# Kernel tuning notes

Measured on AMD Instinct MI355X. Metric: run time of the kernel, lower is better.

Reference implementation:

```python
import jax, jax.numpy as jnp
import numpy as np

INPUT_DIM = 1024
MEMORY_DIM = 512
MEMORY_SIZE = 4096
TOPK = 8


def setup_inputs() -> dict:
    key = jax.random.key(0)
    ks = jax.random.split(key, 7)
    query = jax.random.normal(ks[0], (8, 4096, INPUT_DIM), dtype=jnp.float32)
    memory_keys = jax.random.normal(ks[1], (MEMORY_SIZE, MEMORY_DIM), dtype=jnp.float32)
    memory_values = jax.random.normal(ks[2], (MEMORY_SIZE, MEMORY_DIM), dtype=jnp.float32)
    # nn.Linear-style init (uniform +-1/sqrt(fan_in))
    wq = jax.random.uniform(ks[3], (INPUT_DIM, MEMORY_DIM), jnp.float32, -1.0, 1.0) / np.sqrt(INPUT_DIM)
    bq = jax.random.uniform(ks[4], (MEMORY_DIM,), jnp.float32, -1.0, 1.0) / np.sqrt(INPUT_DIM)
    wo = jax.random.uniform(ks[5], (MEMORY_DIM, INPUT_DIM), jnp.float32, -1.0, 1.0) / np.sqrt(MEMORY_DIM)
    bo = jax.random.uniform(ks[6], (INPUT_DIM,), jnp.float32, -1.0, 1.0) / np.sqrt(MEMORY_DIM)
    return {"query": query, "memory_keys": memory_keys, "memory_values": memory_values,
            "wq": wq, "bq": bq, "wo": wo, "bo": bo}


def reference(query, memory_keys, memory_values, wq, bq, wo, bo):
    B, S, D = query.shape
    # Query projection: [B,S,M]
    q = jnp.einsum('bsd,dm->bsm', query, wq) + bq
    # Scores vs memory keys: [B,S,memory_size] (no expand needed)
    scores = jnp.einsum('bsm,km->bsk', q, memory_keys)
    # Top-k selection + softmax over selected scores
    topk_w, topk_idx = jax.lax.top_k(scores, TOPK)           # [B,S,K]
    topk_w = jax.nn.softmax(topk_w, axis=-1)
    # Gather selected memory values: [B,S,K,M]
    top_vals = memory_values[topk_idx]
    mem_out = jnp.einsum('bskm,bsk->bsm', top_vals, topk_w)  # weighted sum
    out = jnp.einsum('bsm,md->bsd', mem_out, wo) + bo
    return out + query
```

## Files before the change

kernel.cpp:

```cpp
#include <hip/hip_runtime.h>
#include <cstdint>

typedef _Float16 f16;
typedef uint32_t u32;
typedef f16 f16x2 __attribute__((ext_vector_type(2)));
typedef f16 f16x8 __attribute__((ext_vector_type(8)));
typedef float f32x4 __attribute__((ext_vector_type(4)));
typedef float f32x16 __attribute__((ext_vector_type(16)));
typedef u32 u32x4 __attribute__((ext_vector_type(4)));

#define NROWS 32768
#define D_IN 1024
#define M_DIM 512
#define NKEYS 4096
#define KTOP 8

__device__ __forceinline__ u32 umax32(u32 a, u32 b) { return a > b ? a : b; }
__device__ __forceinline__ u32 umin32(u32 a, u32 b) { return a < b ? a : b; }

__device__ __forceinline__ void gload_lds16(const void* src, void* dst) {
  __builtin_amdgcn_global_load_lds(
      (const __attribute__((address_space(1))) uint32_t*)src,
      (__attribute__((address_space(3))) uint32_t*)dst, 16, 0, 0);
}

__global__ void prep_kernel(const float* __restrict__ keys, const float* __restrict__ values,
                            const float* __restrict__ wq, const float* __restrict__ wo,
                            f16* __restrict__ keys_h, f16* __restrict__ values_h,
                            f16* __restrict__ wqT, f16* __restrict__ woT) {
  const int b = blockIdx.x, t = threadIdx.x;
  if (b < 2048) {
    const float* src = (b < 1024) ? keys : values;
    f16* dst = (b < 1024) ? keys_h : values_h;
    const int bb = b & 1023;
    const size_t base = (size_t)bb * 2048 + (size_t)t * 8;
    f32x4 a = *(const f32x4*)(src + base);
    f32x4 c2 = *(const f32x4*)(src + base + 4);
    f16x8 o;
    o[0] = (f16)a[0]; o[1] = (f16)a[1]; o[2] = (f16)a[2]; o[3] = (f16)a[3];
    o[4] = (f16)c2[0]; o[5] = (f16)c2[1]; o[6] = (f16)c2[2]; o[7] = (f16)c2[3];
    *(f16x8*)(dst + base) = o;
    return;
  }
  __shared__ float lds[64][65];
  if (b < 2176) {
    const int tb = b - 2048;
    const int td = tb >> 3, tm = tb & 7;
#pragma unroll
    for (int p = 0; p < 16; ++p) {
      const int d_loc = p * 4 + (t >> 6), m_loc = t & 63;
      lds[d_loc][m_loc] = wq[(size_t)(td * 64 + d_loc) * 512 + tm * 64 + m_loc];
    }
    __syncthreads();
#pragma unroll
    for (int p = 0; p < 16; ++p) {
      const int m_loc = p * 4 + (t >> 6), d_loc = t & 63;
      wqT[(size_t)(tm * 64 + m_loc) * 1024 + td * 64 + d_loc] = (f16)lds[d_loc][m_loc];
    }
  } else {
    const int tb = b - 2176;
    const int tmm = tb >> 4, tod = tb & 15;
#pragma unroll
    for (int p = 0; p < 16; ++p) {
      const int m_loc = p * 4 + (t >> 6), od_loc = t & 63;
      lds[m_loc][od_loc] = wo[(size_t)(tmm * 64 + m_loc) * 1024 + tod * 64 + od_loc];
    }
    __syncthreads();
#pragma unroll
    for (int p = 0; p < 16; ++p) {
      const int od_loc = p * 4 + (t >> 6), m_loc = t & 63;
      woT[(size_t)(tod * 64 + od_loc) * 512 + tmm * 64 + m_loc] = (f16)lds[m_loc][od_loc];
    }
  }
}

__global__ __launch_bounds__(256, 2) void qproj_kernel(
    const float* __restrict__ query, const f16* __restrict__ wqT,
    const float* __restrict__ bq, f16* __restrict__ q_out) {
  __shared__ f16 Atile[32 * 1024];
  const int tid = threadIdx.x;
  const int wave = tid >> 6, lane = tid & 63;
  const int g = lane >> 4, c = lane & 15;
  const int rowbase = blockIdx.x * 64 + wave * 16;
  const int row = rowbase + c;

  f16x8 Breg[32];
  {
    const float* qrow = query + (size_t)row * D_IN;
#pragma unroll
    for (int kk = 0; kk < 32; ++kk) {
      f32x4 lo = *(const f32x4*)(qrow + kk * 32 + g * 8);
      f32x4 hi = *(const f32x4*)(qrow + kk * 32 + g * 8 + 4);
      f16x8 v;
      v[0] = (f16)lo[0]; v[1] = (f16)lo[1]; v[2] = (f16)lo[2]; v[3] = (f16)lo[3];
      v[4] = (f16)hi[0]; v[5] = (f16)hi[1]; v[6] = (f16)hi[2]; v[7] = (f16)hi[3];
      Breg[kk] = v;
    }
  }

  for (int mt = 0; mt < 16; ++mt) {
    __syncthreads();
#pragma unroll
    for (int i2 = 0; i2 < 8; ++i2) {
      const int kr = wave * 8 + i2;
#pragma unroll
      for (int hb = 0; hb < 2; ++hb) {
        const u32 slot = (u32)(hb * 1024 + lane * 16);
        const u32 kb = slot ^ (u32)((kr & 7) << 4);
        const char* src = (const char*)(wqT + (size_t)(mt * 32 + kr) * D_IN) + kb;
        gload_lds16(src, (char*)Atile + kr * 2048 + hb * 1024);
      }
    }
    asm volatile("s_waitcnt vmcnt(0)" ::: "memory");
    __syncthreads();

    f32x4 acc0 = {0.f, 0.f, 0.f, 0.f};
    f32x4 acc1 = {0.f, 0.f, 0.f, 0.f};
#pragma unroll
    for (int kk = 0; kk < 32; ++kk) {
      const u32 base = (u32)(kk * 64 + g * 16);
      {
        const int ml = c;
        const u32 off = (u32)(ml * 2048) + (base ^ (u32)((ml & 7) << 4));
        f16x8 a = *(const f16x8*)((const char*)Atile + off);
        acc0 = __builtin_amdgcn_mfma_f32_16x16x32_f16(a, Breg[kk], acc0, 0, 0, 0);
      }
      {
        const int ml = 16 + c;
        const u32 off = (u32)(ml * 2048) + (base ^ (u32)((ml & 7) << 4));
        f16x8 a = *(const f16x8*)((const char*)Atile + off);
        acc1 = __builtin_amdgcn_mfma_f32_16x16x32_f16(a, Breg[kk], acc1, 0, 0, 0);
      }
    }

    f32x4 bq0 = *(const f32x4*)(bq + mt * 32 + g * 4);
    f32x4 bq1 = *(const f32x4*)(bq + mt * 32 + 16 + g * 4);
    f16* qp = q_out + (size_t)row * M_DIM + mt * 32 + g * 4;
    f16x2 p;
    p[0] = (f16)(acc0[0] + bq0[0]); p[1] = (f16)(acc0[1] + bq0[1]); *(f16x2*)(qp + 0) = p;
    p[0] = (f16)(acc0[2] + bq0[2]); p[1] = (f16)(acc0[3] + bq0[3]); *(f16x2*)(qp + 2) = p;
    p[0] = (f16)(acc1[0] + bq1[0]); p[1] = (f16)(acc1[1] + bq1[1]); *(f16x2*)(qp + 16) = p;
    p[0] = (f16)(acc1[2] + bq1[2]); p[1] = (f16)(acc1[3] + bq1[3]); *(f16x2*)(qp + 18) = p;
  }
}

__global__ __launch_bounds__(256, 2) void scores_topk_kernel(
    const f16* __restrict__ q, const f16* __restrict__ keys_h,
    u32* __restrict__ cand) {
  __shared__ f16 Ktile[2][32 * 512];
  const int tid = threadIdx.x;
  const int wave = tid >> 6, lane = tid & 63;
  const int h = lane >> 5, r32 = lane & 31;
  const int rb = blockIdx.x >> 1, half = blockIdx.x & 1;
  const int rowbase = rb * 128 + wave * 32;
  const int myrow = rowbase + r32;
  const int keybase = half * 2048;

  f16x8 Breg[32];
  {
    const f16* qr = q + (size_t)myrow * M_DIM;
#pragma unroll
    for (int kk = 0; kk < 32; ++kk)
      Breg[kk] = *(const f16x8*)(qr + kk * 16 + h * 8);
  }

  u32 topE[KTOP], topO[KTOP];
#pragma unroll
  for (int j = 0; j < KTOP; ++j) { topE[j] = 0u; topO[j] = 0u; }

  auto stage = [&](int buf, int kt) {
#pragma unroll
    for (int i2 = 0; i2 < 8; ++i2) {
      const int kr = wave * 8 + i2;
      const u32 kb = ((u32)(lane * 16)) ^ ((u32)((kr & 7) << 4));
      const char* src = (const char*)(keys_h + (size_t)(keybase + kt * 32 + kr) * M_DIM) + kb;
      gload_lds16(src, (char*)&Ktile[buf][0] + kr * 1024);
    }
  };

  stage(0, 0);
  asm volatile("s_waitcnt vmcnt(0)" ::: "memory");
  __syncthreads();

  for (int kt = 0; kt < 64; ++kt) {
    const int cur = kt & 1;
    if (kt < 63) stage(cur ^ 1, kt + 1);

    f32x16 accA, accB;
#pragma unroll
    for (int i = 0; i < 16; ++i) { accA[i] = 0.f; accB[i] = 0.f; }
    const char* tileb = (const char*)&Ktile[cur][0];
    __builtin_amdgcn_s_setprio(1);
#pragma unroll
    for (int kk = 0; kk < 32; kk += 2) {
      const u32 swz = (u32)((r32 & 7) << 4);
      const u32 offA = (u32)(r32 * 1024) + ((u32)(kk * 32 + h * 16) ^ swz);
      const u32 offB = (u32)(r32 * 1024) + ((u32)((kk + 1) * 32 + h * 16) ^ swz);
      f16x8 aA = *(const f16x8*)(tileb + offA);
      f16x8 aB = *(const f16x8*)(tileb + offB);
      accA = __builtin_amdgcn_mfma_f32_32x32x16_f16(aA, Breg[kk], accA, 0, 0, 0);
      accB = __builtin_amdgcn_mfma_f32_32x32x16_f16(aB, Breg[kk + 1], accB, 0, 0, 0);
    }
    __builtin_amdgcn_s_setprio(0);

#pragma unroll
    for (int i = 0; i < 16; ++i) {
      const float s = accA[i] + accB[i];
      const u32 kidx = (u32)(keybase + kt * 32 + (i & 3) + 8 * (i >> 2) + 4 * h);
      const int bi = __float_as_int(s);
      const u32 mono = (u32)bi ^ (u32)((bi >> 31) | 0x80000000);
      u32 x = ((mono + 0x800u) & 0xFFFFF000u) | kidx;
      if ((i & 1) == 0) {
#pragma unroll
        for (int j = 0; j < KTOP; ++j) { const u32 nt = umax32(topE[j], x); x = umin32(topE[j], x); topE[j] = nt; }
      } else {
#pragma unroll
        for (int j = 0; j < KTOP; ++j) { const u32 nt = umax32(topO[j], x); x = umin32(topO[j], x); topO[j] = nt; }
      }
    }

    asm volatile("s_waitcnt vmcnt(0)" ::: "memory");
    __syncthreads();
  }

#pragma unroll
  for (int j = 0; j < KTOP; ++j) {
    u32 x = topO[j];
#pragma unroll
    for (int jj = 0; jj < KTOP; ++jj) { const u32 nt = umax32(topE[jj], x); x = umin32(topE[jj], x); topE[jj] = nt; }
  }
  u32 oth[KTOP];
#pragma unroll
  for (int j = 0; j < KTOP; ++j) oth[j] = (u32)__shfl((int)topE[j], lane ^ 32);
#pragma unroll
  for (int j = 0; j < KTOP; ++j) {
    u32 x = oth[j];
#pragma unroll
    for (int jj = 0; jj < KTOP; ++jj) { const u32 nt = umax32(topE[jj], x); x = umin32(topE[jj], x); topE[jj] = nt; }
  }

  if (h == 0) {
    u32* cp = cand + (size_t)myrow * 16 + half * 8;
    u32x4 a, b;
    a.x = topE[0]; a.y = topE[1]; a.z = topE[2]; a.w = topE[3];
    b.x = topE[4]; b.y = topE[5]; b.z = topE[6]; b.w = topE[7];
    *(u32x4*)(cp) = a;
    *(u32x4*)(cp + 4) = b;
  }
}

__global__ __launch_bounds__(256, 4) void merge_gather_kernel(
    const u32* __restrict__ cand, const f16* __restrict__ values_h,
    f16* __restrict__ mem_out) {
  const int tid = threadIdx.x;
  const int wave = tid >> 6, lane = tid & 63;
  const int rowbase = blockIdx.x * 32 + wave * 8;
  const int myrow = rowbase + (lane & 7);

  const u32* cp = cand + (size_t)myrow * 16;
  u32x4 a0 = *(const u32x4*)(cp);
  u32x4 a1 = *(const u32x4*)(cp + 4);
  u32x4 b0 = *(const u32x4*)(cp + 8);
  u32x4 b1 = *(const u32x4*)(cp + 12);
  u32 top[KTOP] = {a0.x, a0.y, a0.z, a0.w, a1.x, a1.y, a1.z, a1.w};
  u32 ins[KTOP] = {b0.x, b0.y, b0.z, b0.w, b1.x, b1.y, b1.z, b1.w};
#pragma unroll
  for (int j = 0; j < KTOP; ++j) {
    u32 x = ins[j];
#pragma unroll
    for (int jj = 0; jj < KTOP; ++jj) { const u32 nt = umax32(top[jj], x); x = umin32(top[jj], x); top[jj] = nt; }
  }

  float w[KTOP]; u32 idx[KTOP];
  {
    float s[KTOP];
#pragma unroll
    for (int j = 0; j < KTOP; ++j) {
      const u32 mono = top[j] & 0xFFFFF000u;
      const u32 bits = (mono & 0x80000000u) ? (mono ^ 0x80000000u) : ~mono;
      s[j] = __int_as_float(bits);
      idx[j] = top[j] & 0xFFFu;
    }
    const float m0 = s[0];
    float sum = 0.f;
#pragma unroll
    for (int j = 0; j < KTOP; ++j) { w[j] = __expf(s[j] - m0); sum += w[j]; }
    const float inv = 1.f / sum;
#pragma unroll
    for (int j = 0; j < KTOP; ++j) w[j] *= inv;
  }

  for (int r = 0; r < 8; ++r) {
    float acc2[8];
#pragma unroll
    for (int e = 0; e < 8; ++e) acc2[e] = 0.f;
#pragma unroll
    for (int j = 0; j < KTOP; ++j) {
      const u32 ix = (u32)__shfl((int)idx[j], r);
      const float wj = __shfl(w[j], r);
      const f16x8 v = *(const f16x8*)(values_h + (size_t)ix * M_DIM + lane * 8);
#pragma unroll
      for (int e = 0; e < 8; ++e) acc2[e] += wj * (float)v[e];
    }
    f16x8 o;
#pragma unroll
    for (int e = 0; e < 8; ++e) o[e] = (f16)acc2[e];
    *(f16x8*)(mem_out + (size_t)(rowbase + r) * M_DIM + lane * 8) = o;
  }
}

__global__ __launch_bounds__(256, 2) void outproj_kernel(
    const f16* __restrict__ mem_h, const f16* __restrict__ woT,
    const float* __restrict__ bo, const float* __restrict__ query,
    float* __restrict__ out) {
  __shared__ f16 Atile[32 * 512];
  const int tid = threadIdx.x;
  const int wave = tid >> 6, lane = tid & 63;
  const int g = lane >> 4, c = lane & 15;
  const int rowbase = blockIdx.x * 64 + wave * 16;
  const int row = rowbase + c;

  f16x8 Breg[16];
  {
    const f16* mr = mem_h + (size_t)row * M_DIM;
#pragma unroll
    for (int kk = 0; kk < 16; ++kk)
      Breg[kk] = *(const f16x8*)(mr + kk * 32 + g * 8);
  }

  for (int mt = 0; mt < 32; ++mt) {
    __syncthreads();
#pragma unroll
    for (int i2 = 0; i2 < 8; ++i2) {
      const int kr = wave * 8 + i2;
      const u32 kb = ((u32)(lane * 16)) ^ ((u32)((kr & 7) << 4));
      const char* src = (const char*)(woT + (size_t)(mt * 32 + kr) * M_DIM) + kb;
      gload_lds16(src, (char*)Atile + kr * 1024);
    }
    asm volatile("s_waitcnt vmcnt(0)" ::: "memory");
    __syncthreads();

    f32x4 acc0 = {0.f, 0.f, 0.f, 0.f};
    f32x4 acc1 = {0.f, 0.f, 0.f, 0.f};
#pragma unroll
    for (int kk = 0; kk < 16; ++kk) {
      const u32 base = (u32)(kk * 64 + g * 16);
      {
        const int ml = c;
        const u32 off = (u32)(ml * 1024) + (base ^ (u32)((ml & 7) << 4));
        f16x8 a = *(const f16x8*)((const char*)Atile + off);
        acc0 = __builtin_amdgcn_mfma_f32_16x16x32_f16(a, Breg[kk], acc0, 0, 0, 0);
      }
      {
        const int ml = 16 + c;
        const u32 off = (u32)(ml * 1024) + (base ^ (u32)((ml & 7) << 4));
        f16x8 a = *(const f16x8*)((const char*)Atile + off);
        acc1 = __builtin_amdgcn_mfma_f32_16x16x32_f16(a, Breg[kk], acc1, 0, 0, 0);
      }
    }

    const int od0 = mt * 32 + g * 4;
    f32x4 bo0 = *(const f32x4*)(bo + od0);
    f32x4 bo1 = *(const f32x4*)(bo + od0 + 16);
    const float* qp = query + (size_t)row * D_IN + od0;
    f32x4 q0 = *(const f32x4*)(qp);
    f32x4 q1 = *(const f32x4*)(qp + 16);
    f32x4 o0, o1;
#pragma unroll
    for (int i = 0; i < 4; ++i) {
      o0[i] = acc0[i] + bo0[i] + q0[i];
      o1[i] = acc1[i] + bo1[i] + q1[i];
    }
    float* op = out + (size_t)row * D_IN + od0;
    *(f32x4*)(op) = o0;
    *(f32x4*)(op + 16) = o1;
  }
}

extern "C" void kernel_launch(void* const* d_in, const int* in_sizes, int n_in,
                              void* d_out, int out_size, void* d_ws, size_t ws_size,
                              hipStream_t stream) {
  (void)in_sizes; (void)n_in; (void)out_size;
  const float* query = (const float*)d_in[0];
  const float* mkeys = (const float*)d_in[1];
  const float* mvals = (const float*)d_in[2];
  const float* wq    = (const float*)d_in[3];
  const float* bq    = (const float*)d_in[4];
  const float* wo    = (const float*)d_in[5];
  const float* bo    = (const float*)d_in[6];
  float* out = (float*)d_out;

  char* ws = (char*)d_ws;
  f16* keys_h   = (f16*)(ws);
  f16* values_h = (f16*)(ws + (4u << 20));
  f16* wqT      = (f16*)(ws + (8u << 20));
  f16* woT      = (f16*)(ws + (9u << 20));
  f16* q_h      = (f16*)(ws + (10u << 20));
  f16* mem_h    = (f16*)(ws + (10u << 20) + (size_t)NROWS * M_DIM * 2);
  u32* cand     = (u32*)(ws + (10u << 20) + 2ull * (size_t)NROWS * M_DIM * 2);
  const size_t need = (10u << 20) + 2ull * (size_t)NROWS * M_DIM * 2
                    + (size_t)NROWS * 16 * 4;
  if (ws_size < need) return;

  prep_kernel<<<2304, 256, 0, stream>>>(mkeys, mvals, wq, wo, keys_h, values_h, wqT, woT);
  qproj_kernel<<<NROWS / 64, 256, 0, stream>>>(query, wqT, bq, q_h);
  scores_topk_kernel<<<(NROWS / 128) * 2, 256, 0, stream>>>(q_h, keys_h, cand);
  merge_gather_kernel<<<NROWS / 32, 256, 0, stream>>>(cand, values_h, mem_h);
  outproj_kernel<<<NROWS / 64, 256, 0, stream>>>(mem_h, woT, bo, query, out);
}
```

Before: 367.3 us.

## Switch scores kernel to 16x16x32 MFMA with 512-thread blocks and fewer registers

The scores/top-k kernel now uses 16x16x32 MFMA tiles, so each wave owns 16 query rows instead of 32 and blocks grow to 512 threads (8 waves). The register-resident query fragment halves from 32 to 16 f16x8 vectors and the accumulators shrink from two f32x16 to two f32x4. The aim is higher occupancy (launch bounds raised to 4 blocks) and less register pressure in the top-k insertion loop. The cost is an extra cross-lane shuffle-merge stage, since top-k lists must now be combined across 4 lane groups instead of 2, and each wave reads the key tile twice per 16 rows instead of once per 32.

```diff
diff --git a/kernel.cpp b/kernel.cpp
--- a/kernel.cpp
+++ b/kernel.cpp
@@ -6,7 +6,6 @@
 typedef f16 f16x2 __attribute__((ext_vector_type(2)));
 typedef f16 f16x8 __attribute__((ext_vector_type(8)));
 typedef float f32x4 __attribute__((ext_vector_type(4)));
-typedef float f32x16 __attribute__((ext_vector_type(16)));
 typedef u32 u32x4 __attribute__((ext_vector_type(4)));
 
 #define NROWS 32768
@@ -144,24 +143,24 @@
   }
 }
 
-__global__ __launch_bounds__(256, 2) void scores_topk_kernel(
+__global__ __launch_bounds__(512, 4) void scores_topk_kernel(
     const f16* __restrict__ q, const f16* __restrict__ keys_h,
     u32* __restrict__ cand) {
   __shared__ f16 Ktile[2][32 * 512];
   const int tid = threadIdx.x;
   const int wave = tid >> 6, lane = tid & 63;
-  const int h = lane >> 5, r32 = lane & 31;
+  const int g = lane >> 4, c = lane & 15;
   const int rb = blockIdx.x >> 1, half = blockIdx.x & 1;
-  const int rowbase = rb * 128 + wave * 32;
-  const int myrow = rowbase + r32;
+  const int rowbase = rb * 128 + wave * 16;
+  const int myrow = rowbase + c;
   const int keybase = half * 2048;
 
-  f16x8 Breg[32];
+  f16x8 Breg[16];
   {
     const f16* qr = q + (size_t)myrow * M_DIM;
 #pragma unroll
-    for (int kk = 0; kk < 32; ++kk)
-      Breg[kk] = *(const f16x8*)(qr + kk * 16 + h * 8);
+    for (int kk = 0; kk < 16; ++kk)
+      Breg[kk] = *(const f16x8*)(qr + kk * 32 + g * 8);
   }
 
   u32 topE[KTOP], topO[KTOP];
@@ -170,8 +169,8 @@
 
   auto stage = [&](int buf, int kt) {
 #pragma unroll
-    for (int i2 = 0; i2 < 8; ++i2) {
-      const int kr = wave * 8 + i2;
+    for (int i2 = 0; i2 < 4; ++i2) {
+      const int kr = wave * 4 + i2;
       const u32 kb = ((u32)(lane * 16)) ^ ((u32)((kr & 7) << 4));
       const char* src = (const char*)(keys_h + (size_t)(keybase + kt * 32 + kr) * M_DIM) + kb;
       gload_lds16(src, (char*)&Ktile[buf][0] + kr * 1024);
@@ -182,38 +181,45 @@
   asm volatile("s_waitcnt vmcnt(0)" ::: "memory");
   __syncthreads();
 
+  const u32 swz = (u32)((c & 7) << 4);
+  const u32 rowb0 = (u32)(c * 1024);
+  const u32 rowb1 = (u32)((c + 16) * 1024);
+
   for (int kt = 0; kt < 64; ++kt) {
     const int cur = kt & 1;
     if (kt < 63) stage(cur ^ 1, kt + 1);
 
-    f32x16 accA, accB;
-#pragma unroll
-    for (int i = 0; i < 16; ++i) { accA[i] = 0.f; accB[i] = 0.f; }
+    f32x4 acc0 = {0.f, 0.f, 0.f, 0.f};
+    f32x4 acc1 = {0.f, 0.f, 0.f, 0.f};
     const char* tileb = (const char*)&Ktile[cur][0];
     __builtin_amdgcn_s_setprio(1);
 #pragma unroll
-    for (int kk = 0; kk < 32; kk += 2) {
-      const u32 swz = (u32)((r32 & 7) << 4);
-      const u32 offA = (u32)(r32 * 1024) + ((u32)(kk * 32 + h * 16) ^ swz);
-      const u32 offB = (u32)(r32 * 1024) + ((u32)((kk + 1) * 32 + h * 16) ^ swz);
-      f16x8 aA = *(const f16x8*)(tileb + offA);
-      f16x8 aB = *(const f16x8*)(tileb + offB);
-      accA = __builtin_amdgcn_mfma_f32_32x32x16_f16(aA, Breg[kk], accA, 0, 0, 0);
-      accB = __builtin_amdgcn_mfma_f32_32x32x16_f16(aB, Breg[kk + 1], accB, 0, 0, 0);
+    for (int kk = 0; kk < 16; ++kk) {
+      const u32 col = ((u32)(kk * 64 + g * 16)) ^ swz;
+      f16x8 a0 = *(const f16x8*)(tileb + rowb0 + col);
+      f16x8 a1 = *(const f16x8*)(tileb + rowb1 + col);
+      acc0 = __builtin_amdgcn_mfma_f32_16x16x32_f16(a0, Breg[kk], acc0, 0, 0, 0);
+      acc1 = __builtin_amdgcn_mfma_f32_16x16x32_f16(a1, Breg[kk], acc1, 0, 0, 0);
     }
     __builtin_amdgcn_s_setprio(0);
 
 #pragma unroll
-    for (int i = 0; i < 16; ++i) {
-      const float s = accA[i] + accB[i];
-      const u32 kidx = (u32)(keybase + kt * 32 + (i & 3) + 8 * (i >> 2) + 4 * h);
-      const int bi = __float_as_int(s);
-      const u32 mono = (u32)bi ^ (u32)((bi >> 31) | 0x80000000);
-      u32 x = ((mono + 0x800u) & 0xFFFFF000u) | kidx;
-      if ((i & 1) == 0) {
+    for (int i = 0; i < 4; ++i) {
+      {
+        const float s = acc0[i];
+        const u32 kidx = (u32)(keybase + kt * 32 + g * 4 + i);
+        const int bi = __float_as_int(s);
+        const u32 mono = (u32)bi ^ (u32)((bi >> 31) | 0x80000000);
+        u32 x = ((mono + 0x800u) & 0xFFFFF000u) | kidx;
 #pragma unroll
         for (int j = 0; j < KTOP; ++j) { const u32 nt = umax32(topE[j], x); x = umin32(topE[j], x); topE[j] = nt; }
-      } else {
+      }
+      {
+        const float s = acc1[i];
+        const u32 kidx = (u32)(keybase + kt * 32 + 16 + g * 4 + i);
+        const int bi = __float_as_int(s);
+        const u32 mono = (u32)bi ^ (u32)((bi >> 31) | 0x80000000);
+        u32 x = ((mono + 0x800u) & 0xFFFFF000u) | kidx;
 #pragma unroll
         for (int j = 0; j < KTOP; ++j) { const u32 nt = umax32(topO[j], x); x = umin32(topO[j], x); topO[j] = nt; }
       }
@@ -229,17 +235,20 @@
 #pragma unroll
     for (int jj = 0; jj < KTOP; ++jj) { const u32 nt = umax32(topE[jj], x); x = umin32(topE[jj], x); topE[jj] = nt; }
   }
-  u32 oth[KTOP];
-#pragma unroll
-  for (int j = 0; j < KTOP; ++j) oth[j] = (u32)__shfl((int)topE[j], lane ^ 32);
-#pragma unroll
-  for (int j = 0; j < KTOP; ++j) {
-    u32 x = oth[j];
-#pragma unroll
-    for (int jj = 0; jj < KTOP; ++jj) { const u32 nt = umax32(topE[jj], x); x = umin32(topE[jj], x); topE[jj] = nt; }
-  }
-
-  if (h == 0) {
+#pragma unroll
+  for (int st = 16; st <= 32; st <<= 1) {
+    u32 oth[KTOP];
+#pragma unroll
+    for (int j = 0; j < KTOP; ++j) oth[j] = (u32)__shfl((int)topE[j], lane ^ st);
+#pragma unroll
+    for (int j = 0; j < KTOP; ++j) {
+      u32 x = oth[j];
+#pragma unroll
+      for (int jj = 0; jj < KTOP; ++jj) { const u32 nt = umax32(topE[jj], x); x = umin32(topE[jj], x); topE[jj] = nt; }
+    }
+  }
+
+  if (g == 0) {
     u32* cp = cand + (size_t)myrow * 16 + half * 8;
     u32x4 a, b;
     a.x = topE[0]; a.y = topE[1]; a.z = topE[2]; a.w = topE[3];
@@ -404,7 +413,7 @@
 
   prep_kernel<<<2304, 256, 0, stream>>>(mkeys, mvals, wq, wo, keys_h, values_h, wqT, woT);
   qproj_kernel<<<NROWS / 64, 256, 0, stream>>>(query, wqT, bq, q_h);
-  scores_topk_kernel<<<(NROWS / 128) * 2, 256, 0, stream>>>(q_h, keys_h, cand);
+  scores_topk_kernel<<<(NROWS / 128) * 2, 512, 0, stream>>>(q_h, keys_h, cand);
   merge_gather_kernel<<<NROWS / 32, 256, 0, stream>>>(cand, values_h, mem_h);
   outproj_kernel<<<NROWS / 64, 256, 0, stream>>>(mem_h, woT, bo, query, out);
 }
```

Result: no change. 364.8 us (-0.7%).

## Software-pipeline top-k insertion behind next tile's MFMA compute

Applied to the files above, without the earlier changes.

Unrolls the key-tile loop by two with two accumulator sets, so the scalar top-k insertion for tile kt-1 is issued after the MFMA chain for tile kt. The aim is to let VALU compare/swap work overlap the matrix-core latency instead of running serially after each tile. The cost is 32 more accumulator registers, which may raise register pressure and lower occupancy.

```diff
diff --git a/kernel.cpp b/kernel.cpp
--- a/kernel.cpp
+++ b/kernel.cpp
@@ -178,34 +178,29 @@
     }
   };
 
-  stage(0, 0);
-  asm volatile("s_waitcnt vmcnt(0)" ::: "memory");
-  __syncthreads();
-
-  for (int kt = 0; kt < 64; ++kt) {
-    const int cur = kt & 1;
-    if (kt < 63) stage(cur ^ 1, kt + 1);
-
-    f32x16 accA, accB;
-#pragma unroll
-    for (int i = 0; i < 16; ++i) { accA[i] = 0.f; accB[i] = 0.f; }
-    const char* tileb = (const char*)&Ktile[cur][0];
+  const u32 swz = (u32)((r32 & 7) << 4);
+  const u32 rowb = (u32)(r32 * 1024);
+
+  auto compute = [&](const char* tileb, f32x16& aA, f32x16& aB) {
+#pragma unroll
+    for (int i = 0; i < 16; ++i) { aA[i] = 0.f; aB[i] = 0.f; }
     __builtin_amdgcn_s_setprio(1);
 #pragma unroll
     for (int kk = 0; kk < 32; kk += 2) {
-      const u32 swz = (u32)((r32 & 7) << 4);
-      const u32 offA = (u32)(r32 * 1024) + ((u32)(kk * 32 + h * 16) ^ swz);
-      const u32 offB = (u32)(r32 * 1024) + ((u32)((kk + 1) * 32 + h * 16) ^ swz);
-      f16x8 aA = *(const f16x8*)(tileb + offA);
-      f16x8 aB = *(const f16x8*)(tileb + offB);
-      accA = __builtin_amdgcn_mfma_f32_32x32x16_f16(aA, Breg[kk], accA, 0, 0, 0);
-      accB = __builtin_amdgcn_mfma_f32_32x32x16_f16(aB, Breg[kk + 1], accB, 0, 0, 0);
+      const u32 offA = rowb + ((u32)(kk * 32 + h * 16) ^ swz);
+      const u32 offB = rowb + ((u32)((kk + 1) * 32 + h * 16) ^ swz);
+      f16x8 fA = *(const f16x8*)(tileb + offA);
+      f16x8 fB = *(const f16x8*)(tileb + offB);
+      aA = __builtin_amdgcn_mfma_f32_32x32x16_f16(fA, Breg[kk], aA, 0, 0, 0);
+      aB = __builtin_amdgcn_mfma_f32_32x32x16_f16(fB, Breg[kk + 1], aB, 0, 0, 0);
     }
     __builtin_amdgcn_s_setprio(0);
-
+  };
+
+  auto topk = [&](const f32x16& aA, const f32x16& aB, int kt) {
 #pragma unroll
     for (int i = 0; i < 16; ++i) {
-      const float s = accA[i] + accB[i];
+      const float s = aA[i] + aB[i];
       const u32 kidx = (u32)(keybase + kt * 32 + (i & 3) + 8 * (i >> 2) + 4 * h);
       const int bi = __float_as_int(s);
       const u32 mono = (u32)bi ^ (u32)((bi >> 31) | 0x80000000);
@@ -218,10 +213,30 @@
         for (int j = 0; j < KTOP; ++j) { const u32 nt = umax32(topO[j], x); x = umin32(topO[j], x); topO[j] = nt; }
       }
     }
-
+  };
+
+  f32x16 accA0, accB0, accA1, accB1;
+#pragma unroll
+  for (int i = 0; i < 16; ++i) { accA1[i] = 0.f; accB1[i] = 0.f; }
+
+  stage(0, 0);
+  asm volatile("s_waitcnt vmcnt(0)" ::: "memory");
+  __syncthreads();
+
+#pragma unroll 1
+  for (int kt = 0; kt < 64; kt += 2) {
+    stage(1, kt + 1);
+    compute((const char*)&Ktile[0][0], accA0, accB0);
+    if (kt > 0) topk(accA1, accB1, kt - 1);
     asm volatile("s_waitcnt vmcnt(0)" ::: "memory");
     __syncthreads();
-  }
+    if (kt + 2 < 64) stage(0, kt + 2);
+    compute((const char*)&Ktile[1][0], accA1, accB1);
+    topk(accA0, accB0, kt);
+    asm volatile("s_waitcnt vmcnt(0)" ::: "memory");
+    __syncthreads();
+  }
+  topk(accA1, accB1, 63);
 
 #pragma unroll
   for (int j = 0; j < KTOP; ++j) {
```

Result: slower. 457.5 us (+24.6%).

## Defer top-k insertion one tile to overlap with MFMA; split outproj columns across blocks

Applied to the files above, without the earlier changes.

The scores kernel now saves each tile's summed scores and runs the top-k insertion for the previous tile after issuing the current tile's MFMAs. This lets the compare-swap VALU work overlap with matrix-core work, and it merges the even/odd top lists into a single list. The outproj kernel splits the output columns into two halves handled by separate blocks, doubling the grid and raising the occupancy hint to 4. The cost is extra registers for the saved scores, a longer serial insertion chain per element, and each outproj block reloading its A rows twice.

```diff
diff --git a/kernel.cpp b/kernel.cpp
--- a/kernel.cpp
+++ b/kernel.cpp
@@ -164,9 +164,10 @@
       Breg[kk] = *(const f16x8*)(qr + kk * 16 + h * 8);
   }
 
-  u32 topE[KTOP], topO[KTOP];
-#pragma unroll
-  for (int j = 0; j < KTOP; ++j) { topE[j] = 0u; topO[j] = 0u; }
+  u32 top[KTOP];
+#pragma unroll
+  for (int j = 0; j < KTOP; ++j) top[j] = 0u;
+  float sPrev[16];
 
   auto stage = [&](int buf, int kt) {
 #pragma unroll
@@ -178,10 +179,26 @@
     }
   };
 
+  auto topk_prev = [&](int ktm1) {
+#pragma unroll
+    for (int i = 0; i < 16; ++i) {
+      const u32 kidx = (u32)(keybase + ktm1 * 32 + (i & 3) + 8 * (i >> 2) + 4 * h);
+      const int bi = __float_as_int(sPrev[i]);
+      const u32 mono = (u32)bi ^ (u32)((bi >> 31) | 0x80000000);
+      u32 x = ((mono + 0x800u) & 0xFFFFF000u) | kidx;
+#pragma unroll
+      for (int j = 0; j < KTOP; ++j) { const u32 nt = umax32(top[j], x); x = umin32(top[j], x); top[j] = nt; }
+    }
+  };
+
   stage(0, 0);
   asm volatile("s_waitcnt vmcnt(0)" ::: "memory");
   __syncthreads();
 
+  const u32 swz = (u32)((r32 & 7) << 4);
+  const u32 rowb = (u32)(r32 * 1024);
+
+#pragma unroll 1
   for (int kt = 0; kt < 64; ++kt) {
     const int cur = kt & 1;
     if (kt < 63) stage(cur ^ 1, kt + 1);
@@ -193,57 +210,40 @@
     __builtin_amdgcn_s_setprio(1);
 #pragma unroll
     for (int kk = 0; kk < 32; kk += 2) {
-      const u32 swz = (u32)((r32 & 7) << 4);
-      const u32 offA = (u32)(r32 * 1024) + ((u32)(kk * 32 + h * 16) ^ swz);
-      const u32 offB = (u32)(r32 * 1024) + ((u32)((kk + 1) * 32 + h * 16) ^ swz);
-      f16x8 aA = *(const f16x8*)(tileb + offA);
-      f16x8 aB = *(const f16x8*)(tileb + offB);
-      accA = __builtin_amdgcn_mfma_f32_32x32x16_f16(aA, Breg[kk], accA, 0, 0, 0);
-      accB = __builtin_amdgcn_mfma_f32_32x32x16_f16(aB, Breg[kk + 1], accB, 0, 0, 0);
+      const u32 offA = rowb + ((u32)(kk * 32 + h * 16) ^ swz);
+      const u32 offB = rowb + ((u32)((kk + 1) * 32 + h * 16) ^ swz);
+      f16x8 fA = *(const f16x8*)(tileb + offA);
+      f16x8 fB = *(const f16x8*)(tileb + offB);
+      accA = __builtin_amdgcn_mfma_f32_32x32x16_f16(fA, Breg[kk], accA, 0, 0, 0);
+      accB = __builtin_amdgcn_mfma_f32_32x32x16_f16(fB, Breg[kk + 1], accB, 0, 0, 0);
     }
     __builtin_amdgcn_s_setprio(0);
 
-#pragma unroll
-    for (int i = 0; i < 16; ++i) {
-      const float s = accA[i] + accB[i];
-      const u32 kidx = (u32)(keybase + kt * 32 + (i & 3) + 8 * (i >> 2) + 4 * h);
-      const int bi = __float_as_int(s);
-      const u32 mono = (u32)bi ^ (u32)((bi >> 31) | 0x80000000);
-      u32 x = ((mono + 0x800u) & 0xFFFFF000u) | kidx;
-      if ((i & 1) == 0) {
-#pragma unroll
-        for (int j = 0; j < KTOP; ++j) { const u32 nt = umax32(topE[j], x); x = umin32(topE[j], x); topE[j] = nt; }
-      } else {
-#pragma unroll
-        for (int j = 0; j < KTOP; ++j) { const u32 nt = umax32(topO[j], x); x = umin32(topO[j], x); topO[j] = nt; }
-      }
-    }
+    if (kt > 0) topk_prev(kt - 1);
+
+#pragma unroll
+    for (int i = 0; i < 16; ++i) sPrev[i] = accA[i] + accB[i];
 
     asm volatile("s_waitcnt vmcnt(0)" ::: "memory");
     __syncthreads();
   }
-
-#pragma unroll
-  for (int j = 0; j < KTOP; ++j) {
-    u32 x = topO[j];
-#pragma unroll
-    for (int jj = 0; jj < KTOP; ++jj) { const u32 nt = umax32(topE[jj], x); x = umin32(topE[jj], x); topE[jj] = nt; }
-  }
+  topk_prev(63);
+
   u32 oth[KTOP];
 #pragma unroll
-  for (int j = 0; j < KTOP; ++j) oth[j] = (u32)__shfl((int)topE[j], lane ^ 32);
+  for (int j = 0; j < KTOP; ++j) oth[j] = (u32)__shfl((int)top[j], lane ^ 32);
 #pragma unroll
   for (int j = 0; j < KTOP; ++j) {
     u32 x = oth[j];
 #pragma unroll
-    for (int jj = 0; jj < KTOP; ++jj) { const u32 nt = umax32(topE[jj], x); x = umin32(topE[jj], x); topE[jj] = nt; }
+    for (int jj = 0; jj < KTOP; ++jj) { const u32 nt = umax32(top[jj], x); x = umin32(top[jj], x); top[jj] = nt; }
   }
 
   if (h == 0) {
     u32* cp = cand + (size_t)myrow * 16 + half * 8;
     u32x4 a, b;
-    a.x = topE[0]; a.y = topE[1]; a.z = topE[2]; a.w = topE[3];
-    b.x = topE[4]; b.y = topE[5]; b.z = topE[6]; b.w = topE[7];
+    a.x = top[0]; a.y = top[1]; a.z = top[2]; a.w = top[3];
+    b.x = top[4]; b.y = top[5]; b.z = top[6]; b.w = top[7];
     *(u32x4*)(cp) = a;
     *(u32x4*)(cp + 4) = b;
   }
@@ -309,7 +309,7 @@
   }
 }
 
-__global__ __launch_bounds__(256, 2) void outproj_kernel(
+__global__ __launch_bounds__(256, 4) void outproj_kernel(
     const f16* __restrict__ mem_h, const f16* __restrict__ woT,
     const float* __restrict__ bo, const float* __restrict__ query,
     float* __restrict__ out) {
@@ -317,7 +317,8 @@
   const int tid = threadIdx.x;
   const int wave = tid >> 6, lane = tid & 63;
   const int g = lane >> 4, c = lane & 15;
-  const int rowbase = blockIdx.x * 64 + wave * 16;
+  const int rbk = blockIdx.x >> 1, mh = blockIdx.x & 1;
+  const int rowbase = rbk * 64 + wave * 16;
   const int row = rowbase + c;
 
   f16x8 Breg[16];
@@ -328,7 +329,7 @@
       Breg[kk] = *(const f16x8*)(mr + kk * 32 + g * 8);
   }
 
-  for (int mt = 0; mt < 32; ++mt) {
+  for (int mt = mh * 16; mt < mh * 16 + 16; ++mt) {
     __syncthreads();
 #pragma unroll
     for (int i2 = 0; i2 < 8; ++i2) {
@@ -406,5 +407,5 @@
   qproj_kernel<<<NROWS / 64, 256, 0, stream>>>(query, wqT, bq, q_h);
   scores_topk_kernel<<<(NROWS / 128) * 2, 256, 0, stream>>>(q_h, keys_h, cand);
   merge_gather_kernel<<<NROWS / 32, 256, 0, stream>>>(cand, values_h, mem_h);
-  outproj_kernel<<<NROWS / 64, 256, 0, stream>>>(mem_h, woT, bo, query, out);
-}
+  outproj_kernel<<<(NROWS / 64) * 2, 256, 0, stream>>>(mem_h, woT, bo, query, out);
+}
```

After: 350.7 us. 1.05x faster.
